# Optimization experiments

Measured on AMD Instinct MI355X. Metric: run time of the kernel, lower is better.

The kernel has to match this reference:

```python
import jax, jax.numpy as jnp
import numpy as np

B, C, Q, T, D = 16, 6, 256, 256, 256
NUM_IDS = 300
IMG_H = IMG_W = 512


def setup_inputs() -> dict:
    key = jax.random.key(0)
    ks = jax.random.split(key, 8)
    det_tokens = jax.random.normal(ks[0], (B, C, Q, D), jnp.float32)
    det_scores = jax.random.uniform(ks[1], (B, C, Q), jnp.float32)
    det_boxes = jax.random.uniform(ks[2], (B, C, Q, 4), jnp.float32)
    assoc = jax.nn.softmax(jax.random.normal(ks[3], (B, C, Q, T), jnp.float32), axis=-1)
    cam_mask = jax.random.uniform(ks[4], (B, C)) < 0.9
    target_mask = jax.random.uniform(ks[5], (B, C, Q)) < 0.5
    ids = jax.random.randint(ks[6], (B, C, Q), 0, NUM_IDS)
    boxes = jax.random.uniform(ks[7], (B, C, Q, 4), jnp.float32) * IMG_W
    return {"det_tokens": det_tokens, "det_scores": det_scores, "det_boxes": det_boxes,
            "assoc": assoc, "boxes": boxes, "cam_mask": cam_mask,
            "target_mask": target_mask, "ids": ids, "img_h": IMG_H, "img_w": IMG_W}


def _masked_mean(x, m):
    w = m.astype(x.dtype)
    return (x * w).sum() / jnp.maximum(w.sum(), 1.0)


def _pack(ids, target_mask, cam_mask, q_count):
    # Vectorized version of _query_ids_from_targets: stable-compact valid targets
    # to the front of the query axis (preserves original order, as boolean indexing does).
    order = jnp.argsort(jnp.where(target_mask, 0, 1), axis=-1, stable=True)  # valid first
    sids = jnp.take_along_axis(ids, order, axis=-1)[..., :q_count]
    count = target_mask.sum(axis=-1)  # [B,C]
    qvalid = (jnp.arange(q_count)[None, None, :] < count[..., None]) & cam_mask[..., None]
    qids = jnp.where(qvalid, sids, -1)
    return qids, qvalid, order


def reference(det_tokens, det_scores, det_boxes, assoc, boxes, cam_mask, target_mask, ids, img_h, img_w):
    Bq, Cc, Qn, Tn = assoc.shape
    qids, qvalid, order = _pack(ids, target_mask, cam_mask, Qn)

    # det_norm
    det_norm = jnp.mean(det_tokens ** 2)

    # detector supervision (masked BCE on scores + masked L1 on boxes)
    norm = jnp.array([img_w, img_h, img_w, img_h], det_boxes.dtype)
    box_gt = boxes / norm  # [B,C,maxT,4]
    sboxes = jnp.take_along_axis(box_gt, order[..., None], axis=2)[:, :, :Qn]
    obj_target = qvalid.astype(det_scores.dtype)
    box_target = jnp.where(qvalid[..., None], jnp.clip(sboxes, 0.0, 1.0), 0.0)
    p = jnp.clip(det_scores, 1e-6, 1.0 - 1e-6)
    bce = -(obj_target * jnp.log(p) + (1.0 - obj_target) * jnp.log1p(-p))
    cam3 = jnp.broadcast_to(cam_mask[:, :, None], bce.shape)
    score_loss = _masked_mean(bce, cam3)
    box_loss = _masked_mean(jnp.abs(det_boxes - box_target),
                            jnp.broadcast_to(qvalid[..., None], det_boxes.shape))
    det_supervision = score_loss + box_loss

    # assoc entropy (masked by camera validity)
    logp_full = jnp.log(jnp.maximum(assoc, 1e-8))
    entropy = -(logp_full * assoc).sum(-1)  # [B,C,Q]
    assoc_entropy_loss = _masked_mean(entropy, jnp.broadcast_to(cam_mask[:, :, None], entropy.shape))

    # assoc supervised NLL over track slots
    slots = jnp.remainder(jnp.maximum(qids, 0), Tn)  # [B,C,Q]
    nll = -jnp.take_along_axis(logp_full, slots[..., None], axis=-1)[..., 0]
    assoc_pair_loss = _masked_mean(nll, qvalid)

    # cross-view consistency: broadcasted id-equality replaces quadruple python loop
    eq = qids[:, :, None, :, None] == qids[:, None, :, None, :]       # [B,c1,c2,q1,q2]
    pv = qvalid[:, :, None, :, None] & qvalid[:, None, :, None, :]
    tri = jnp.triu(jnp.ones((Cc, Cc), bool), 1)[None, :, :, None, None]  # c1 < c2
    M = (eq & pv & tri).astype(assoc.dtype)
    cnt = M.sum(-1)  # [B,c1,c2,q1]
    peer = jnp.einsum('bcdqp,bdpt->bcdqt', M, assoc) / jnp.maximum(cnt, 1.0)[..., None]
    ref = assoc[:, :, None, :, :]
    term = jnp.mean((ref - peer) ** 2, axis=-1)  # per-pair MSE over track slots
    assoc_consistency = _masked_mean(term, cnt > 0)

    total = det_norm + det_supervision + assoc_entropy_loss + assoc_pair_loss + assoc_consistency
    return total, det_norm, det_supervision, assoc_entropy_loss, assoc_pair_loss, assoc_consistency
```

## Files before the change

kernel.cpp:

```cpp
#include <hip/hip_runtime.h>
#include <math.h>

#define BB 16
#define CC 6
#define QQ 256
#define TT 256
#define DD 256
#define NPAIR 15
#define NBC (BB * CC)
#define CONS_BLOCKS (BB * NPAIR * 4)
#define PACK_BLOCKS NBC
#define BIG_BLOCKS (NBC * 8)
#define MAIN_BLOCKS (CONS_BLOCKS + PACK_BLOCKS + BIG_BLOCKS)


__device__ __forceinline__ float block_sum256(float v, float* s_red) {
    #pragma unroll
    for (int off = 32; off > 0; off >>= 1) v += __shfl_xor(v, off, 64);
    __syncthreads();
    if ((threadIdx.x & 63) == 0) s_red[threadIdx.x >> 6] = v;
    __syncthreads();
    return s_red[0] + s_red[1] + s_red[2] + s_red[3];
}

__device__ __forceinline__ float2 block_sum256x2(float a, float b, float2* s_red2) {
    #pragma unroll
    for (int off = 32; off > 0; off >>= 1) {
        a += __shfl_xor(a, off, 64);
        b += __shfl_xor(b, off, 64);
    }
    __syncthreads();
    if ((threadIdx.x & 63) == 0) s_red2[threadIdx.x >> 6] = make_float2(a, b);
    __syncthreads();
    float2 r;
    r.x = s_red2[0].x + s_red2[1].x + s_red2[2].x + s_red2[3].x;
    r.y = s_red2[0].y + s_red2[1].y + s_red2[2].y + s_red2[3].y;
    return r;
}

__device__ __forceinline__ int read_bool(const void* p, int idx, int fmt) {
    if (fmt == 2) return ((const float*)p)[idx] != 0.0f;
    if (fmt == 1) return ((const unsigned char*)p)[idx] != 0;
    return ((const int*)p)[idx] != 0;
}

__device__ __forceinline__ int detect_fmt(const void* tm_raw, int* s_cf, int* s_cm) {
    const int t = threadIdx.x;
    if (t == 0) { *s_cf = 0; *s_cm = 0; }
    __syncthreads();
    uint4 w = ((const uint4*)tm_raw)[t];
    unsigned int u4[4] = {w.x, w.y, w.z, w.w};
    int cf = 0, cm = 0;
    #pragma unroll
    for (int k = 0; k < 4; k++) {
        cf += ((u4[k] >> 24) == 0x3Fu);
        cm += ((u4[k] & 0xFFFFFF00u) != 0u);
    }
    if (cf) atomicAdd(s_cf, cf);
    if (cm) atomicAdd(s_cm, cm);
    __syncthreads();
    return (*s_cf > 16) ? 2 : ((*s_cm > 0) ? 1 : 0);
}

__device__ __forceinline__ int block_pack(const void* tm_raw,
                                          const int* __restrict__ ids,
                                          int bc, int fmt, int cam,
                                          int* s_sids, int* s_wsum,
                                          int* s_out) {
    const int t = threadIdx.x, lane = t & 63, wv = t >> 6;
    const int tm = read_bool(tm_raw, bc * QQ + t, fmt);
    int v = tm;
    #pragma unroll
    for (int off = 1; off < 64; off <<= 1) {
        int u = __shfl_up(v, off, 64);
        if (lane >= off) v += u;
    }
    if (lane == 63) s_wsum[wv] = v;
    __syncthreads();
    const int count = s_wsum[0] + s_wsum[1] + s_wsum[2] + s_wsum[3];
    int woff = 0;
    #pragma unroll
    for (int k = 0; k < 3; k++) woff += (k < wv) ? s_wsum[k] : 0;
    const int excl = woff + v - tm;
    const int rank = tm ? excl : (count + (t - excl));
    s_sids[rank] = ids[bc * QQ + t];
    __syncthreads();
    s_out[t] = (t < count && cam) ? s_sids[t] : -1;
    __syncthreads();
    return count;
}

__global__ __launch_bounds__(256)
void k_main(const float4* __restrict__ tok,
            const float* __restrict__ assoc,
            const float* __restrict__ det_scores,
            const float* __restrict__ det_boxes,
            const float* __restrict__ boxes,
            const void* __restrict__ cam_raw,
            const void* __restrict__ tm_raw,
            const int* __restrict__ ids,
            const int* __restrict__ img_h_p,
            const int* __restrict__ img_w_p,
            float* __restrict__ packPart,
            float* __restrict__ bigPart,
            float* __restrict__ consPart) {
    const int blk = blockIdx.x;
    const int t = threadIdx.x, lane = t & 63, wv = t >> 6;
    __shared__ int s_cf, s_cm;
    __shared__ float2 s_red2[4];

    if (blk >= CONS_BLOCKS + PACK_BLOCKS) {
        const int bb = blk - (CONS_BLOCKS + PACK_BLOCKS);
        const int bc = bb >> 3;
        const long base = (long)bc * 16384 + (long)(bb & 7) * 2048 + t;
        const float4* asc = (const float4*)assoc;
        const int fmt = detect_fmt(tm_raw, &s_cf, &s_cm);
        const int cam = read_bool(cam_raw, bc, fmt);

        float ss = 0.0f, ent = 0.0f;
        #pragma unroll
        for (int h = 0; h < 2; h++) {
            const long o = base + h * 1024;
            float4 t0 = tok[o], t1 = tok[o + 256], t2 = tok[o + 512], t3 = tok[o + 768];
            float4 a0 = asc[o], a1 = asc[o + 256], a2 = asc[o + 512], a3 = asc[o + 768];
            ss += t0.x * t0.x + t0.y * t0.y + t0.z * t0.z + t0.w * t0.w
                + t1.x * t1.x + t1.y * t1.y + t1.z * t1.z + t1.w * t1.w
                + t2.x * t2.x + t2.y * t2.y + t2.z * t2.z + t2.w * t2.w
                + t3.x * t3.x + t3.y * t3.y + t3.z * t3.z + t3.w * t3.w;
            if (cam) {
                ent -= a0.x * __logf(fmaxf(a0.x, 1e-8f)) + a0.y * __logf(fmaxf(a0.y, 1e-8f))
                     + a0.z * __logf(fmaxf(a0.z, 1e-8f)) + a0.w * __logf(fmaxf(a0.w, 1e-8f));
                ent -= a1.x * __logf(fmaxf(a1.x, 1e-8f)) + a1.y * __logf(fmaxf(a1.y, 1e-8f))
                     + a1.z * __logf(fmaxf(a1.z, 1e-8f)) + a1.w * __logf(fmaxf(a1.w, 1e-8f));
                ent -= a2.x * __logf(fmaxf(a2.x, 1e-8f)) + a2.y * __logf(fmaxf(a2.y, 1e-8f))
                     + a2.z * __logf(fmaxf(a2.z, 1e-8f)) + a2.w * __logf(fmaxf(a2.w, 1e-8f));
                ent -= a3.x * __logf(fmaxf(a3.x, 1e-8f)) + a3.y * __logf(fmaxf(a3.y, 1e-8f))
                     + a3.z * __logf(fmaxf(a3.z, 1e-8f)) + a3.w * __logf(fmaxf(a3.w, 1e-8f));
            }
        }
        float2 r = block_sum256x2(ss, ent, s_red2);
        if (t == 0) { bigPart[bb * 2] = r.x; bigPart[bb * 2 + 1] = r.y; }

    } else if (blk >= CONS_BLOCKS) {
        const int bc = blk - CONS_BLOCKS;
        __shared__ int s_sids[QQ], s_qid[QQ], s_wsum[4];
        const int fmt = detect_fmt(tm_raw, &s_cf, &s_cm);
        const int cam = read_bool(cam_raw, bc, fmt);
        const int count = block_pack(tm_raw, ids, bc, fmt, cam, s_sids, s_wsum, s_qid);
        const int tm = read_bool(tm_raw, bc * QQ + t, fmt);
        int v = tm;
        #pragma unroll
        for (int off = 1; off < 64; off <<= 1) {
            int u = __shfl_up(v, off, 64);
            if (lane >= off) v += u;
        }
        int woff = 0;
        #pragma unroll
        for (int k = 0; k < 3; k++) woff += (k < wv) ? s_wsum[k] : 0;
        const int excl = woff + v - tm;
        const int rank = tm ? excl : (count + (t - excl));

        const int j = t;
        const int qv = (j < count) && cam;
        const int qid = s_qid[j];

        float score_sum = 0.0f, box_sum = 0.0f, pair_sum = 0.0f;
        if (cam) {
            float p = det_scores[(size_t)bc * QQ + j];
            p = fminf(fmaxf(p, 1e-6f), 1.0f - 1e-6f);
            score_sum = (j < count) ? -__logf(p) : -__logf(1.0f - p);
        }
        if (qv) {
            int slot = qid & (TT - 1);
            float a = assoc[((size_t)bc * QQ + j) * TT + slot];
            pair_sum = -__logf(fmaxf(a, 1e-8f));
        }
        if (tm && cam) {
            const int jj = rank;
            const float iw = (float)img_w_p[0], ih = (float)img_h_p[0];
            const float* bx = boxes + ((size_t)bc * QQ + t) * 4;
            const float* db = det_boxes + ((size_t)bc * QQ + jj) * 4;
            float b0 = fminf(fmaxf(bx[0] / iw, 0.0f), 1.0f);
            float b1 = fminf(fmaxf(bx[1] / ih, 0.0f), 1.0f);
            float b2 = fminf(fmaxf(bx[2] / iw, 0.0f), 1.0f);
            float b3 = fminf(fmaxf(bx[3] / ih, 0.0f), 1.0f);
            box_sum = fabsf(db[0] - b0) + fabsf(db[1] - b1) +
                      fabsf(db[2] - b2) + fabsf(db[3] - b3);
        }
        float2 r1 = block_sum256x2(score_sum, box_sum, s_red2);
        float2 r2 = block_sum256x2(pair_sum, 0.0f, s_red2);
        if (t == 0) {
            float* row = packPart + bc * 8;
            row[0] = r1.x; row[1] = r1.y; row[2] = r2.x;
            row[3] = cam ? (float)count : 0.0f;
            row[4] = (float)cam;
        }

    } else {
        const int cb = blk;
        const int qg = cb & 3;
        const int bp = cb >> 2;
        const int b = bp / NPAIR;
        int pi = bp % NPAIR;
        int c = 0, d = 1;
        {
            int k = pi;
            for (c = 0; c < CC - 1; c++) {
                int span = CC - 1 - c;
                if (k < span) { d = c + 1 + k; break; }
                k -= span;
            }
        }
        __shared__ int s_sids[QQ], s_qc[QQ], s_qd[QQ], s_wsum[4];
        const int fmt = detect_fmt(tm_raw, &s_cf, &s_cm);
        const int cam_c = read_bool(cam_raw, b * CC + c, fmt);
        const int cam_d = read_bool(cam_raw, b * CC + d, fmt);
        block_pack(tm_raw, ids, b * CC + c, fmt, cam_c, s_sids, s_wsum, s_qc);
        block_pack(tm_raw, ids, b * CC + d, fmt, cam_d, s_sids, s_wsum, s_qd);

        const int qd0 = s_qd[lane];
        const int qd1 = s_qd[64 + lane];
        const int qd2 = s_qd[128 + lane];
        const int qd3 = s_qd[192 + lane];
        int idarr[16];
        #pragma unroll
        for (int qi = 0; qi < 16; qi++) idarr[qi] = s_qc[qg * 64 + wv * 16 + qi];

        const float4* assoc_c = (const float4*)(assoc + (size_t)(b * CC + c) * QQ * TT);
        const float4* assoc_d = (const float4*)(assoc + (size_t)(b * CC + d) * QQ * TT);

        float tot = 0.0f, nval = 0.0f;
        #pragma unroll 4
        for (int qi = 0; qi < 16; qi++) {
            const int id = idarr[qi];
            if (id < 0) continue;
            unsigned long long m0 = __ballot(qd0 == id);
            unsigned long long m1 = __ballot(qd1 == id);
            unsigned long long m2 = __ballot(qd2 == id);
            unsigned long long m3 = __ballot(qd3 == id);
            int cnt = __popcll(m0) + __popcll(m1) + __popcll(m2) + __popcll(m3);
            if (cnt == 0) continue;
            const int q = qg * 64 + wv * 16 + qi;
            float4 r = assoc_c[(size_t)q * (TT / 4) + lane];
            float ax = 0.0f, ay = 0.0f, az = 0.0f, aw = 0.0f;
            unsigned long long mm[4] = {m0, m1, m2, m3};
            #pragma unroll
            for (int kk = 0; kk < 4; kk++) {
                unsigned long long m = mm[kk];
                while (m) {
                    int p = kk * 64 + __builtin_ctzll(m);
                    m &= m - 1;
                    float4 vv = assoc_d[(size_t)p * (TT / 4) + lane];
                    ax += vv.x; ay += vv.y; az += vv.z; aw += vv.w;
                }
            }
            float inv = 1.0f / (float)cnt;
            float dx = r.x - ax * inv, dy = r.y - ay * inv;
            float dz = r.z - az * inv, dw = r.w - aw * inv;
            tot += dx * dx + dy * dy + dz * dz + dw * dw;
            nval += 1.0f;
        }
        float2 r2 = block_sum256x2(tot, nval, s_red2);
        if (t == 0) {
            consPart[cb * 2] = r2.x * (1.0f / TT);
            consPart[cb * 2 + 1] = r2.y;
        }
    }
}

__global__ __launch_bounds__(256)
void k_fin(const float* __restrict__ packPart, const float2* __restrict__ bigPart,
           const float2* __restrict__ consPart, float* __restrict__ out) {
    const int t = threadIdx.x;
    __shared__ float s_red[4];
    float sc = 0, bx = 0, pr = 0, qv = 0, cm = 0;
    if (t < NBC) {
        const float* row = packPart + t * 8;
        sc = row[0]; bx = row[1]; pr = row[2]; qv = row[3]; cm = row[4];
    }
    float ss = 0, ent = 0;
    #pragma unroll
    for (int k = 0; k < BIG_BLOCKS / 256; k++) {
        float2 v = bigPart[k * 256 + t];
        ss += v.x; ent += v.y;
    }
    float cons = 0, nval = 0;
    for (int i = t; i < CONS_BLOCKS; i += 256) {
        float2 v = consPart[i];
        cons += v.x; nval += v.y;
    }
    sc = block_sum256(sc, s_red);
    bx = block_sum256(bx, s_red);
    pr = block_sum256(pr, s_red);
    qv = block_sum256(qv, s_red);
    cm = block_sum256(cm, s_red);
    ss = block_sum256(ss, s_red);
    ent = block_sum256(ent, s_red);
    cons = block_sum256(cons, s_red);
    nval = block_sum256(nval, s_red);
    if (t == 0) {
        float det_norm = ss / (float)((long)BB * CC * QQ * DD);
        float denom_cam = fmaxf(cm * (float)QQ, 1.0f);
        float score_loss = sc / denom_cam;
        float box_loss = bx / fmaxf(4.0f * qv, 1.0f);
        float det_sup = score_loss + box_loss;
        float ent_loss = ent / denom_cam;
        float pair_loss = pr / fmaxf(qv, 1.0f);
        float cons_loss = cons / fmaxf(nval, 1.0f);
        out[0] = det_norm + det_sup + ent_loss + pair_loss + cons_loss;
        out[1] = det_norm;
        out[2] = det_sup;
        out[3] = ent_loss;
        out[4] = pair_loss;
        out[5] = cons_loss;
    }
}

extern "C" void kernel_launch(void* const* d_in, const int* in_sizes, int n_in,
                              void* d_out, int out_size, void* d_ws, size_t ws_size,
                              hipStream_t stream) {
    const float* det_tokens = (const float*)d_in[0];
    const float* det_scores = (const float*)d_in[1];
    const float* det_boxes  = (const float*)d_in[2];
    const float* assoc      = (const float*)d_in[3];
    const float* boxes      = (const float*)d_in[4];
    const void*  cam_raw    = d_in[5];
    const void*  tm_raw     = d_in[6];
    const int*   ids        = (const int*)d_in[7];
    const int*   img_h      = (const int*)d_in[8];
    const int*   img_w      = (const int*)d_in[9];

    char* ws = (char*)d_ws;
    float* packPart = (float*)(ws + 0);
    float* bigPart  = (float*)(ws + 4096);
    float* consPart = (float*)(ws + 16384);

    k_main<<<MAIN_BLOCKS, 256, 0, stream>>>((const float4*)det_tokens, assoc,
                                            det_scores, det_boxes, boxes,
                                            cam_raw, tm_raw, ids, img_h, img_w,
                                            packPart, bigPart, consPart);
    k_fin<<<1, 256, 0, stream>>>(packPart, (const float2*)bigPart,
                                 (const float2*)consPart, (float*)d_out);
}
```

Before: 111.9 us.

## Fold pack-loss blocks into consistency blocks and cap registers for occupancy

Drops the separate per-camera pack blocks. Three chosen camera-pair consistency blocks, pairs (0,1), (2,3) and (4,5), now compute the score, box and pair losses from the pack results they already hold, so no pack work is repeated. It also adds launch_bounds(256,8), turns the big-reduction loop into four non-unrolled iterations with fewer loads in flight, and reads query ids from shared memory instead of a register array. The aim is fewer blocks and higher occupancy, at the cost of less memory-level parallelism in the streaming reduction and extra tail work on a few consistency blocks.

```diff
diff --git a/kernel.cpp b/kernel.cpp
--- a/kernel.cpp
+++ b/kernel.cpp
@@ -9,9 +9,8 @@
 #define NPAIR 15
 #define NBC (BB * CC)
 #define CONS_BLOCKS (BB * NPAIR * 4)
-#define PACK_BLOCKS NBC
 #define BIG_BLOCKS (NBC * 8)
-#define MAIN_BLOCKS (CONS_BLOCKS + PACK_BLOCKS + BIG_BLOCKS)
+#define MAIN_BLOCKS (CONS_BLOCKS + BIG_BLOCKS)
 
 
 __device__ __forceinline__ float block_sum256(float v, float* s_red) {
@@ -62,11 +61,13 @@
     return (*s_cf > 16) ? 2 : ((*s_cm > 0) ? 1 : 0);
 }
 
-__device__ __forceinline__ int block_pack(const void* tm_raw,
-                                          const int* __restrict__ ids,
-                                          int bc, int fmt, int cam,
-                                          int* s_sids, int* s_wsum,
-                                          int* s_out) {
+struct PackRes { int count; int rank; int tm; };
+
+__device__ __forceinline__ PackRes block_pack(const void* tm_raw,
+                                              const int* __restrict__ ids,
+                                              int bc, int fmt, int cam,
+                                              int* s_sids, int* s_wsum,
+                                              int* s_out) {
     const int t = threadIdx.x, lane = t & 63, wv = t >> 6;
     const int tm = read_bool(tm_raw, bc * QQ + t, fmt);
     int v = tm;
@@ -87,10 +88,57 @@
     __syncthreads();
     s_out[t] = (t < count && cam) ? s_sids[t] : -1;
     __syncthreads();
-    return count;
-}
-
-__global__ __launch_bounds__(256)
+    PackRes r; r.count = count; r.rank = rank; r.tm = tm;
+    return r;
+}
+
+__device__ __forceinline__ void pack_losses(int bc, PackRes pr, int cam,
+                                            const int* s_qe,
+                                            const float* __restrict__ det_scores,
+                                            const float* __restrict__ det_boxes,
+                                            const float* __restrict__ boxes,
+                                            const float* __restrict__ assoc,
+                                            const int* __restrict__ img_h_p,
+                                            const int* __restrict__ img_w_p,
+                                            float2* s_red2,
+                                            float* __restrict__ packPart) {
+    const int t = threadIdx.x;
+    const int j = t;
+    const int qid = s_qe[j];
+    float score_sum = 0.0f, box_sum = 0.0f, pair_sum = 0.0f;
+    if (cam) {
+        float p = det_scores[(size_t)bc * QQ + j];
+        p = fminf(fmaxf(p, 1e-6f), 1.0f - 1e-6f);
+        score_sum = (j < pr.count) ? -__logf(p) : -__logf(1.0f - p);
+    }
+    if (qid >= 0) {
+        int slot = qid & (TT - 1);
+        float a = assoc[((size_t)bc * QQ + j) * TT + slot];
+        pair_sum = -__logf(fmaxf(a, 1e-8f));
+    }
+    if (pr.tm && cam) {
+        const int jj = pr.rank;
+        const float iw = (float)img_w_p[0], ih = (float)img_h_p[0];
+        const float* bx = boxes + ((size_t)bc * QQ + t) * 4;
+        const float* db = det_boxes + ((size_t)bc * QQ + jj) * 4;
+        float b0 = fminf(fmaxf(bx[0] / iw, 0.0f), 1.0f);
+        float b1 = fminf(fmaxf(bx[1] / ih, 0.0f), 1.0f);
+        float b2 = fminf(fmaxf(bx[2] / iw, 0.0f), 1.0f);
+        float b3 = fminf(fmaxf(bx[3] / ih, 0.0f), 1.0f);
+        box_sum = fabsf(db[0] - b0) + fabsf(db[1] - b1) +
+                  fabsf(db[2] - b2) + fabsf(db[3] - b3);
+    }
+    float2 r1 = block_sum256x2(score_sum, box_sum, s_red2);
+    float2 r2 = block_sum256x2(pair_sum, 0.0f, s_red2);
+    if (t == 0) {
+        float* row = packPart + bc * 8;
+        row[0] = r1.x; row[1] = r1.y; row[2] = r2.x;
+        row[3] = cam ? (float)pr.count : 0.0f;
+        row[4] = (float)cam;
+    }
+}
+
+__global__ __launch_bounds__(256, 8)
 void k_main(const float4* __restrict__ tok,
             const float* __restrict__ assoc,
             const float* __restrict__ det_scores,
@@ -109,8 +157,8 @@
     __shared__ int s_cf, s_cm;
     __shared__ float2 s_red2[4];
 
-    if (blk >= CONS_BLOCKS + PACK_BLOCKS) {
-        const int bb = blk - (CONS_BLOCKS + PACK_BLOCKS);
+    if (blk >= CONS_BLOCKS) {
+        const int bb = blk - CONS_BLOCKS;
         const int bc = bb >> 3;
         const long base = (long)bc * 16384 + (long)(bb & 7) * 2048 + t;
         const float4* asc = (const float4*)assoc;
@@ -118,96 +166,35 @@
         const int cam = read_bool(cam_raw, bc, fmt);
 
         float ss = 0.0f, ent = 0.0f;
-        #pragma unroll
-        for (int h = 0; h < 2; h++) {
-            const long o = base + h * 1024;
-            float4 t0 = tok[o], t1 = tok[o + 256], t2 = tok[o + 512], t3 = tok[o + 768];
-            float4 a0 = asc[o], a1 = asc[o + 256], a2 = asc[o + 512], a3 = asc[o + 768];
+        #pragma unroll 1
+        for (int h = 0; h < 4; h++) {
+            const long o = base + h * 512;
+            float4 t0 = tok[o], t1 = tok[o + 256];
+            float4 a0 = asc[o], a1 = asc[o + 256];
             ss += t0.x * t0.x + t0.y * t0.y + t0.z * t0.z + t0.w * t0.w
-                + t1.x * t1.x + t1.y * t1.y + t1.z * t1.z + t1.w * t1.w
-                + t2.x * t2.x + t2.y * t2.y + t2.z * t2.z + t2.w * t2.w
-                + t3.x * t3.x + t3.y * t3.y + t3.z * t3.z + t3.w * t3.w;
+                + t1.x * t1.x + t1.y * t1.y + t1.z * t1.z + t1.w * t1.w;
             if (cam) {
                 ent -= a0.x * __logf(fmaxf(a0.x, 1e-8f)) + a0.y * __logf(fmaxf(a0.y, 1e-8f))
                      + a0.z * __logf(fmaxf(a0.z, 1e-8f)) + a0.w * __logf(fmaxf(a0.w, 1e-8f));
                 ent -= a1.x * __logf(fmaxf(a1.x, 1e-8f)) + a1.y * __logf(fmaxf(a1.y, 1e-8f))
                      + a1.z * __logf(fmaxf(a1.z, 1e-8f)) + a1.w * __logf(fmaxf(a1.w, 1e-8f));
-                ent -= a2.x * __logf(fmaxf(a2.x, 1e-8f)) + a2.y * __logf(fmaxf(a2.y, 1e-8f))
-                     + a2.z * __logf(fmaxf(a2.z, 1e-8f)) + a2.w * __logf(fmaxf(a2.w, 1e-8f));
-                ent -= a3.x * __logf(fmaxf(a3.x, 1e-8f)) + a3.y * __logf(fmaxf(a3.y, 1e-8f))
-                     + a3.z * __logf(fmaxf(a3.z, 1e-8f)) + a3.w * __logf(fmaxf(a3.w, 1e-8f));
             }
         }
         float2 r = block_sum256x2(ss, ent, s_red2);
         if (t == 0) { bigPart[bb * 2] = r.x; bigPart[bb * 2 + 1] = r.y; }
-
-    } else if (blk >= CONS_BLOCKS) {
-        const int bc = blk - CONS_BLOCKS;
-        __shared__ int s_sids[QQ], s_qid[QQ], s_wsum[4];
-        const int fmt = detect_fmt(tm_raw, &s_cf, &s_cm);
-        const int cam = read_bool(cam_raw, bc, fmt);
-        const int count = block_pack(tm_raw, ids, bc, fmt, cam, s_sids, s_wsum, s_qid);
-        const int tm = read_bool(tm_raw, bc * QQ + t, fmt);
-        int v = tm;
-        #pragma unroll
-        for (int off = 1; off < 64; off <<= 1) {
-            int u = __shfl_up(v, off, 64);
-            if (lane >= off) v += u;
-        }
-        int woff = 0;
-        #pragma unroll
-        for (int k = 0; k < 3; k++) woff += (k < wv) ? s_wsum[k] : 0;
-        const int excl = woff + v - tm;
-        const int rank = tm ? excl : (count + (t - excl));
-
-        const int j = t;
-        const int qv = (j < count) && cam;
-        const int qid = s_qid[j];
-
-        float score_sum = 0.0f, box_sum = 0.0f, pair_sum = 0.0f;
-        if (cam) {
-            float p = det_scores[(size_t)bc * QQ + j];
-            p = fminf(fmaxf(p, 1e-6f), 1.0f - 1e-6f);
-            score_sum = (j < count) ? -__logf(p) : -__logf(1.0f - p);
-        }
-        if (qv) {
-            int slot = qid & (TT - 1);
-            float a = assoc[((size_t)bc * QQ + j) * TT + slot];
-            pair_sum = -__logf(fmaxf(a, 1e-8f));
-        }
-        if (tm && cam) {
-            const int jj = rank;
-            const float iw = (float)img_w_p[0], ih = (float)img_h_p[0];
-            const float* bx = boxes + ((size_t)bc * QQ + t) * 4;
-            const float* db = det_boxes + ((size_t)bc * QQ + jj) * 4;
-            float b0 = fminf(fmaxf(bx[0] / iw, 0.0f), 1.0f);
-            float b1 = fminf(fmaxf(bx[1] / ih, 0.0f), 1.0f);
-            float b2 = fminf(fmaxf(bx[2] / iw, 0.0f), 1.0f);
-            float b3 = fminf(fmaxf(bx[3] / ih, 0.0f), 1.0f);
-            box_sum = fabsf(db[0] - b0) + fabsf(db[1] - b1) +
-                      fabsf(db[2] - b2) + fabsf(db[3] - b3);
-        }
-        float2 r1 = block_sum256x2(score_sum, box_sum, s_red2);
-        float2 r2 = block_sum256x2(pair_sum, 0.0f, s_red2);
-        if (t == 0) {
-            float* row = packPart + bc * 8;
-            row[0] = r1.x; row[1] = r1.y; row[2] = r2.x;
-            row[3] = cam ? (float)count : 0.0f;
-            row[4] = (float)cam;
-        }
 
     } else {
         const int cb = blk;
         const int qg = cb & 3;
         const int bp = cb >> 2;
         const int b = bp / NPAIR;
-        int pi = bp % NPAIR;
+        const int pi = bp % NPAIR;
         int c = 0, d = 1;
         {
-            int k = pi;
-            for (c = 0; c < CC - 1; c++) {
-                int span = CC - 1 - c;
-                if (k < span) { d = c + 1 + k; break; }
+            int k = pi, cc;
+            for (cc = 0; cc < CC - 1; cc++) {
+                int span = CC - 1 - cc;
+                if (k < span) { c = cc; d = cc + 1 + k; break; }
                 k -= span;
             }
         }
@@ -215,24 +202,19 @@
         const int fmt = detect_fmt(tm_raw, &s_cf, &s_cm);
         const int cam_c = read_bool(cam_raw, b * CC + c, fmt);
         const int cam_d = read_bool(cam_raw, b * CC + d, fmt);
-        block_pack(tm_raw, ids, b * CC + c, fmt, cam_c, s_sids, s_wsum, s_qc);
-        block_pack(tm_raw, ids, b * CC + d, fmt, cam_d, s_sids, s_wsum, s_qd);
+        PackRes prc = block_pack(tm_raw, ids, b * CC + c, fmt, cam_c, s_sids, s_wsum, s_qc);
+        PackRes prd = block_pack(tm_raw, ids, b * CC + d, fmt, cam_d, s_sids, s_wsum, s_qd);
 
         const int qd0 = s_qd[lane];
         const int qd1 = s_qd[64 + lane];
         const int qd2 = s_qd[128 + lane];
         const int qd3 = s_qd[192 + lane];
-        int idarr[16];
-        #pragma unroll
-        for (int qi = 0; qi < 16; qi++) idarr[qi] = s_qc[qg * 64 + wv * 16 + qi];
-
         const float4* assoc_c = (const float4*)(assoc + (size_t)(b * CC + c) * QQ * TT);
         const float4* assoc_d = (const float4*)(assoc + (size_t)(b * CC + d) * QQ * TT);
 
         float tot = 0.0f, nval = 0.0f;
-        #pragma unroll 4
         for (int qi = 0; qi < 16; qi++) {
-            const int id = idarr[qi];
+            const int id = s_qc[qg * 64 + wv * 16 + qi];
             if (id < 0) continue;
             unsigned long long m0 = __ballot(qd0 == id);
             unsigned long long m1 = __ballot(qd1 == id);
@@ -265,6 +247,13 @@
             consPart[cb * 2] = r2.x * (1.0f / TT);
             consPart[cb * 2 + 1] = r2.y;
         }
+
+        if (qg == 0 && (pi == 0 || pi == 9 || pi == 14)) {
+            pack_losses(b * CC + c, prc, cam_c, s_qc, det_scores, det_boxes,
+                        boxes, assoc, img_h_p, img_w_p, s_red2, packPart);
+            pack_losses(b * CC + d, prd, cam_d, s_qd, det_scores, det_boxes,
+                        boxes, assoc, img_h_p, img_w_p, s_red2, packPart);
+        }
     }
 }
 
```

After: 114.4 us. +2.2%, slower.
